# Optimization experiments

Measured on AMD Instinct MI355X. Metric: run time of the kernel, lower is better.

The kernel has to match this reference:

```python
import jax, jax.numpy as jnp
import numpy as np

N_NODES = 100000
N_EDGES = 1000000
HIDDEN = 64
NUM_CONVS = 3
EPS = 0.0  # GINEConv eps, not trained


def setup_inputs() -> dict:
    key = jax.random.key(0)
    ks = jax.random.split(key, 8)
    z = jax.random.randint(ks[0], (N_NODES,), 0, 100, dtype=jnp.int32)
    edge_index = jax.random.randint(ks[1], (2, N_EDGES), 0, N_NODES, dtype=jnp.int32)
    edge_attr = jax.random.normal(ks[2], (N_EDGES, HIDDEN), dtype=jnp.float32)
    node_emb = jax.random.normal(ks[3], (100, HIDDEN), dtype=jnp.float32)
    s = 1.0 / np.sqrt(HIDDEN)
    W1 = jax.random.uniform(ks[4], (NUM_CONVS, HIDDEN, HIDDEN), jnp.float32, -s, s)
    b1 = jax.random.uniform(ks[5], (NUM_CONVS, HIDDEN), jnp.float32, -s, s)
    W2 = jax.random.uniform(ks[6], (NUM_CONVS, HIDDEN, HIDDEN), jnp.float32, -s, s)
    b2 = jax.random.uniform(ks[7], (NUM_CONVS, HIDDEN), jnp.float32, -s, s)
    return {"node_emb": node_emb, "W1": W1, "b1": b1, "W2": W2, "b2": b2,
            "edge_attr": edge_attr, "z": z, "edge_index": edge_index}


def reference(node_emb, W1, b1, W2, b2, edge_attr, z, edge_index):
    x = node_emb[z]  # [N, H]
    src = edge_index[0]  # x_j (source, message sender)
    dst = edge_index[1]  # aggregation target i
    n = x.shape[0]
    for i in range(NUM_CONVS):
        # message: relu(x_j + edge_attr), scatter-add to target nodes
        msg = jax.nn.relu(x[src] + edge_attr)          # [E, H]
        agg = jax.ops.segment_sum(msg, dst, num_segments=n)  # [N, H]
        out = agg + (1.0 + EPS) * x
        # 2-layer MLP: Linear -> relu -> Linear (no act on last layer)
        h = jax.nn.relu(out @ W1[i].T + b1[i])
        h = h @ W2[i].T + b2[i]
        if i < NUM_CONVS - 1:
            h = jax.nn.relu(h)  # encoder-level activation between convs
        h = h + x  # short_cut residual
        x = h
    return x
```

## Files before the change

### kernel.cpp

```cpp
#include <hip/hip_runtime.h>

#define N_NODES 100000
#define N_EDGES 1000000
#define HID 64
#define SCAN_B 1024
#define SCAN_NB ((N_NODES + SCAN_B - 1) / SCAN_B)

__global__ __launch_bounds__(256) void gather_kernel(
    const float* __restrict__ node_emb, const int* __restrict__ z,
    float* __restrict__ x)
{
    int t = blockIdx.x * 256 + threadIdx.x;
    int n = t >> 4, c = t & 15;
    if (n >= N_NODES) return;
    int zi = z[n];
    float4 v = ((const float4*)(node_emb + (size_t)zi * HID))[c];
    ((float4*)(x + (size_t)n * HID))[c] = v;
}

__global__ __launch_bounds__(256) void hist_kernel(
    const int* __restrict__ dst, int* __restrict__ offs)
{
    int e = blockIdx.x * 256 + threadIdx.x;
    if (e < N_EDGES) atomicAdd(&offs[dst[e]], 1);
}

__global__ __launch_bounds__(1024) void scan1_kernel(
    int* __restrict__ offs, int* __restrict__ bsum)
{
    __shared__ int wsum[16];
    int tid = threadIdx.x, lane = tid & 63, wid = tid >> 6;
    int i = blockIdx.x * SCAN_B + tid;
    int v = (i < N_NODES) ? offs[i] : 0;
    int s = v;
#pragma unroll
    for (int d = 1; d < 64; d <<= 1) {
        int t = __shfl_up(s, (unsigned)d, 64);
        if (lane >= d) s += t;
    }
    if (lane == 63) wsum[wid] = s;
    __syncthreads();
    if (wid == 0) {
        int w = (lane < 16) ? wsum[lane] : 0;
#pragma unroll
        for (int d = 1; d < 16; d <<= 1) {
            int t = __shfl_up(w, (unsigned)d, 64);
            if (lane >= d) w += t;
        }
        if (lane < 16) wsum[lane] = w;
    }
    __syncthreads();
    int woff = (wid == 0) ? 0 : wsum[wid - 1];
    if (i < N_NODES) offs[i] = woff + s - v;
    if (tid == 1023) bsum[blockIdx.x] = wsum[15];
}

__global__ __launch_bounds__(128) void scan2_kernel(int* __restrict__ bsum)
{
    __shared__ int ws[2];
    int tid = threadIdx.x, lane = tid & 63, wid = tid >> 6;
    int v = (tid < SCAN_NB) ? bsum[tid] : 0;
    int s = v;
#pragma unroll
    for (int d = 1; d < 64; d <<= 1) {
        int t = __shfl_up(s, (unsigned)d, 64);
        if (lane >= d) s += t;
    }
    if (lane == 63) ws[wid] = s;
    __syncthreads();
    int add = (wid == 1) ? ws[0] : 0;
    if (tid < SCAN_NB) bsum[tid] = add + s - v;
}

__global__ __launch_bounds__(1024) void scan3_kernel(
    int* __restrict__ offs, const int* __restrict__ bsum)
{
    int i = blockIdx.x * SCAN_B + threadIdx.x;
    if (i < N_NODES) {
        int v = offs[i] + bsum[blockIdx.x];
        atomicExch(&offs[i], v);
    }
}

__global__ __launch_bounds__(256) void fill_kernel(
    const int* __restrict__ src, const int* __restrict__ dst,
    int* __restrict__ offs, int2* __restrict__ eid2)
{
    int e = blockIdx.x * 256 + threadIdx.x;
    if (e < N_EDGES) {
        int d = dst[e];
        int pos = atomicAdd(&offs[d], 1);
        eid2[pos] = make_int2(e, src[e]);
    }
}

__global__ __launch_bounds__(256) void sort_kernel(
    const int* __restrict__ offs, int2* __restrict__ eid2)
{
    int gt = blockIdx.x * 256 + threadIdx.x;
    int n = gt >> 6;
    int lane = threadIdx.x & 63;
    if (n >= N_NODES) return;
    int start = (n == 0) ? 0 : offs[n - 1];
    int end = offs[n];
    int deg = end - start;
    if (deg <= 1 || deg > 64) return;
    int ke = 0x7fffffff, vs = 0;
    if (lane < deg) { int2 t = eid2[start + lane]; ke = t.x; vs = t.y; }
#pragma unroll
    for (int k = 2; k <= 64; k <<= 1) {
        for (int j = k >> 1; j > 0; j >>= 1) {
            int partner = lane ^ j;
            int ke2 = __shfl(ke, partner, 64);
            int vs2 = __shfl(vs, partner, 64);
            bool up = ((lane & k) == 0);
            bool takemin = ((lane < partner) == up);
            bool sw = takemin ? (ke2 < ke) : (ke2 > ke);
            if (sw) { ke = ke2; vs = vs2; }
        }
    }
    if (lane < deg) eid2[start + lane] = make_int2(ke, vs);
}

template<int FIRST>
__global__ __launch_bounds__(256) void agg_kernel(
    const float* __restrict__ x, const float* __restrict__ ea,
    float* __restrict__ eap, const int2* __restrict__ eid2,
    int* __restrict__ srcs, const int* __restrict__ offs,
    float* __restrict__ agg)
{
    int gt = blockIdx.x * 256 + threadIdx.x;
    int n = gt >> 6;
    if (n >= N_NODES) return;
    int lane = threadIdx.x & 63;
    int g = lane >> 4, c4 = lane & 15;
    int nu = __builtin_amdgcn_readfirstlane(n);
    int start = (nu == 0) ? 0 : offs[nu - 1];
    int end = offs[nu];
    float4 acc = make_float4(0.f, 0.f, 0.f, 0.f);
    for (int i = start + g; i < end; i += 4) {
        int sidx;
        float4 e4;
        if (FIRST) {
            int2 p = eid2[i];
            sidx = p.y;
            if (c4 == 0) srcs[i] = sidx;
            e4 = ((const float4*)(ea + (size_t)p.x * HID))[c4];
            ((float4*)(eap + (size_t)i * HID))[c4] = e4;
        } else {
            sidx = srcs[i];
            e4 = ((const float4*)(eap + (size_t)i * HID))[c4];
        }
        float4 x4 = ((const float4*)(x + (size_t)sidx * HID))[c4];
        acc.x += fmaxf(x4.x + e4.x, 0.f);
        acc.y += fmaxf(x4.y + e4.y, 0.f);
        acc.z += fmaxf(x4.z + e4.z, 0.f);
        acc.w += fmaxf(x4.w + e4.w, 0.f);
    }
    acc.x += __shfl_xor(acc.x, 16, 64);
    acc.y += __shfl_xor(acc.y, 16, 64);
    acc.z += __shfl_xor(acc.z, 16, 64);
    acc.w += __shfl_xor(acc.w, 16, 64);
    acc.x += __shfl_xor(acc.x, 32, 64);
    acc.y += __shfl_xor(acc.y, 32, 64);
    acc.z += __shfl_xor(acc.z, 32, 64);
    acc.w += __shfl_xor(acc.w, 32, 64);
    if (g == 0) ((float4*)(agg + (size_t)n * HID))[c4] = acc;
}

#define REP16(M) M(0) M(1) M(2) M(3) M(4) M(5) M(6) M(7) \
                 M(8) M(9) M(10) M(11) M(12) M(13) M(14) M(15)

__global__ __launch_bounds__(256, 2) void mlp_kernel(
    const float* __restrict__ agg,
    const float* __restrict__ W1, const float* __restrict__ b1,
    const float* __restrict__ W2, const float* __restrict__ b2,
    float* __restrict__ x, int last_relu)
{
    __shared__ float sW1[HID * HID];
    __shared__ float sW2T[HID * HID];
    __shared__ float sb1[HID];
    int tid = threadIdx.x;
    for (int idx = tid; idx < HID * HID; idx += 256) {
        sW1[idx] = W1[idx];
        int r = idx >> 6, col = idx & 63;
        sW2T[col * HID + r] = W2[idx];
    }
    if (tid < HID) sb1[tid] = b1[tid];
    __syncthreads();

    int n = blockIdx.x * 256 + tid;
    if (n >= N_NODES) return;

    const float4* ap = (const float4*)(agg + (size_t)n * HID);
    const float4* xp = (const float4*)(x + (size_t)n * HID);
    const float4* b2p = (const float4*)b2;

#define DECL_IN(k) float4 in##k; { float4 a = ap[k], b = xp[k]; \
    in##k.x = a.x + b.x; in##k.y = a.y + b.y; \
    in##k.z = a.z + b.z; in##k.w = a.w + b.w; }
    REP16(DECL_IN)
#undef DECL_IN

#define DECL_O(k) float4 o##k = b2p[k];
    REP16(DECL_O)
#undef DECL_O

    for (int j = 0; j < HID; ++j) {
        const float4* w1p = (const float4*)(sW1 + j * HID);
        float a0 = 0.f, a1 = 0.f, a2 = 0.f, a3 = 0.f;
#define DOT4(k, acc) { float4 w = w1p[k]; \
    acc += in##k.x * w.x + in##k.y * w.y + in##k.z * w.z + in##k.w * w.w; }
        DOT4(0, a0)  DOT4(1, a1)  DOT4(2, a2)  DOT4(3, a3)
        DOT4(4, a0)  DOT4(5, a1)  DOT4(6, a2)  DOT4(7, a3)
        DOT4(8, a0)  DOT4(9, a1)  DOT4(10, a2) DOT4(11, a3)
        DOT4(12, a0) DOT4(13, a1) DOT4(14, a2) DOT4(15, a3)
#undef DOT4
        float h = fmaxf((a0 + a1) + (a2 + a3) + sb1[j], 0.f);
        const float4* w2p = (const float4*)(sW2T + j * HID);
#define AXPY(k) { float4 w = w2p[k]; \
    o##k.x += h * w.x; o##k.y += h * w.y; \
    o##k.z += h * w.z; o##k.w += h * w.w; }
        REP16(AXPY)
#undef AXPY
    }

    float4* orow = (float4*)(x + (size_t)n * HID);
#define STORE(k) { float4 xv = xp[k]; float4 r; \
    r.x = (last_relu ? fmaxf(o##k.x, 0.f) : o##k.x) + xv.x; \
    r.y = (last_relu ? fmaxf(o##k.y, 0.f) : o##k.y) + xv.y; \
    r.z = (last_relu ? fmaxf(o##k.z, 0.f) : o##k.z) + xv.z; \
    r.w = (last_relu ? fmaxf(o##k.w, 0.f) : o##k.w) + xv.w; \
    orow[k] = r; }
    REP16(STORE)
#undef STORE
}

extern "C" void kernel_launch(void* const* d_in, const int* in_sizes, int n_in,
                              void* d_out, int out_size, void* d_ws, size_t ws_size,
                              hipStream_t stream) {
    const float* node_emb = (const float*)d_in[0];
    const float* W1 = (const float*)d_in[1];
    const float* b1 = (const float*)d_in[2];
    const float* W2 = (const float*)d_in[3];
    const float* b2 = (const float*)d_in[4];
    const float* ea = (const float*)d_in[5];
    const int* z = (const int*)d_in[6];
    const int* ei = (const int*)d_in[7];
    const int* src = ei;
    const int* dst = ei + N_EDGES;

    float* x = (float*)d_out;
    float* eap = (float*)d_ws;
    float* agg = eap + (size_t)N_EDGES * HID;
    int2* eid2 = (int2*)(agg + (size_t)N_NODES * HID);
    int* offs = (int*)(eid2 + N_EDGES);
    int* bsum = offs + N_NODES;
    int* srcs = bsum + 128;

    const int eb = (N_EDGES + 255) / 256;
    const int gather_blocks = (N_NODES * 16) / 256;
    const int nodewave_blocks = (N_NODES * 64) / 256;
    const int mlp_blocks = (N_NODES + 255) / 256;

    hipMemsetAsync(offs, 0, N_NODES * sizeof(int), stream);
    gather_kernel<<<gather_blocks, 256, 0, stream>>>(node_emb, z, x);
    hist_kernel<<<eb, 256, 0, stream>>>(dst, offs);
    scan1_kernel<<<SCAN_NB, SCAN_B, 0, stream>>>(offs, bsum);
    scan2_kernel<<<1, 128, 0, stream>>>(bsum);
    scan3_kernel<<<SCAN_NB, SCAN_B, 0, stream>>>(offs, bsum);
    fill_kernel<<<eb, 256, 0, stream>>>(src, dst, offs, eid2);
    sort_kernel<<<nodewave_blocks, 256, 0, stream>>>(offs, eid2);

    agg_kernel<1><<<nodewave_blocks, 256, 0, stream>>>(x, ea, eap, eid2, srcs, offs, agg);
    mlp_kernel<<<mlp_blocks, 256, 0, stream>>>(
        agg, W1, b1, W2, b2, x, 1);
    for (int conv = 1; conv < 3; ++conv) {
        agg_kernel<0><<<nodewave_blocks, 256, 0, stream>>>(x, ea, eap, eid2, srcs, offs, agg);
        mlp_kernel<<<mlp_blocks, 256, 0, stream>>>(
            agg, W1 + conv * HID * HID, b1 + conv * HID,
            W2 + conv * HID * HID, b2 + conv * HID,
            x, conv < 2 ? 1 : 0);
    }
}
```

Measured before the change: 992.0 us.

## Drop permuted edge-attr copy; gather edge attrs directly with wave-shuffled indices

Stops materializing a CSR-permuted copy of edge_attr (256MB write plus reread) and the srcs array in the first conv. Every conv now gathers edge_attr rows by original edge id, and the wave loads up to 64 (edge id, src) pairs at once and broadcasts them via shuffles instead of per-iteration index loads. The gather and histogram kernels are also merged into one launch. The cost is random row gathers from edge_attr in all three convs instead of streaming contiguous reads in two of them.

Result: faster. 942.6 us (-5.0%).

```diff
diff --git a/kernel.cpp b/kernel.cpp
--- a/kernel.cpp
+++ b/kernel.cpp
@@ -5,24 +5,24 @@
 #define HID 64
 #define SCAN_B 1024
 #define SCAN_NB ((N_NODES + SCAN_B - 1) / SCAN_B)
-
-__global__ __launch_bounds__(256) void gather_kernel(
+#define GATHER_BLOCKS ((N_NODES * 16) / 256)
+#define HIST_BLOCKS ((N_EDGES + 255) / 256)
+
+__global__ __launch_bounds__(256) void prep_kernel(
     const float* __restrict__ node_emb, const int* __restrict__ z,
-    float* __restrict__ x)
-{
-    int t = blockIdx.x * 256 + threadIdx.x;
-    int n = t >> 4, c = t & 15;
-    if (n >= N_NODES) return;
-    int zi = z[n];
-    float4 v = ((const float4*)(node_emb + (size_t)zi * HID))[c];
-    ((float4*)(x + (size_t)n * HID))[c] = v;
-}
-
-__global__ __launch_bounds__(256) void hist_kernel(
-    const int* __restrict__ dst, int* __restrict__ offs)
-{
-    int e = blockIdx.x * 256 + threadIdx.x;
-    if (e < N_EDGES) atomicAdd(&offs[dst[e]], 1);
+    float* __restrict__ x, const int* __restrict__ dst, int* __restrict__ offs)
+{
+    if (blockIdx.x < GATHER_BLOCKS) {
+        int t = blockIdx.x * 256 + threadIdx.x;
+        int n = t >> 4, c = t & 15;
+        if (n >= N_NODES) return;
+        int zi = z[n];
+        float4 v = ((const float4*)(node_emb + (size_t)zi * HID))[c];
+        ((float4*)(x + (size_t)n * HID))[c] = v;
+    } else {
+        int e = (blockIdx.x - GATHER_BLOCKS) * 256 + threadIdx.x;
+        if (e < N_EDGES) atomicAdd(&offs[dst[e]], 1);
+    }
 }
 
 __global__ __launch_bounds__(1024) void scan1_kernel(
@@ -122,11 +122,9 @@
     if (lane < deg) eid2[start + lane] = make_int2(ke, vs);
 }
 
-template<int FIRST>
 __global__ __launch_bounds__(256) void agg_kernel(
     const float* __restrict__ x, const float* __restrict__ ea,
-    float* __restrict__ eap, const int2* __restrict__ eid2,
-    int* __restrict__ srcs, const int* __restrict__ offs,
+    const int2* __restrict__ eid2, const int* __restrict__ offs,
     float* __restrict__ agg)
 {
     int gt = blockIdx.x * 256 + threadIdx.x;
@@ -137,21 +135,29 @@
     int nu = __builtin_amdgcn_readfirstlane(n);
     int start = (nu == 0) ? 0 : offs[nu - 1];
     int end = offs[nu];
+    int deg = end - start;
+    int2 my = make_int2(0, 0);
+    if (lane < deg) my = eid2[start + lane];
     float4 acc = make_float4(0.f, 0.f, 0.f, 0.f);
-    for (int i = start + g; i < end; i += 4) {
-        int sidx;
-        float4 e4;
-        if (FIRST) {
-            int2 p = eid2[i];
-            sidx = p.y;
-            if (c4 == 0) srcs[i] = sidx;
-            e4 = ((const float4*)(ea + (size_t)p.x * HID))[c4];
-            ((float4*)(eap + (size_t)i * HID))[c4] = e4;
-        } else {
-            sidx = srcs[i];
-            e4 = ((const float4*)(eap + (size_t)i * HID))[c4];
+    int dmax = deg < 64 ? deg : 64;
+    int iters = (dmax + 3) >> 2;
+    for (int j = 0; j < iters; ++j) {
+        int k = g + 4 * j;
+        int eidx = __shfl(my.x, k, 64);
+        int sidx = __shfl(my.y, k, 64);
+        if (k < dmax) {
+            float4 e4 = ((const float4*)(ea + (size_t)eidx * HID))[c4];
+            float4 x4 = ((const float4*)(x + (size_t)sidx * HID))[c4];
+            acc.x += fmaxf(x4.x + e4.x, 0.f);
+            acc.y += fmaxf(x4.y + e4.y, 0.f);
+            acc.z += fmaxf(x4.z + e4.z, 0.f);
+            acc.w += fmaxf(x4.w + e4.w, 0.f);
         }
-        float4 x4 = ((const float4*)(x + (size_t)sidx * HID))[c4];
+    }
+    for (int i = start + 64 + g; i < end; i += 4) {
+        int2 p = eid2[i];
+        float4 e4 = ((const float4*)(ea + (size_t)p.x * HID))[c4];
+        float4 x4 = ((const float4*)(x + (size_t)p.y * HID))[c4];
         acc.x += fmaxf(x4.x + e4.x, 0.f);
         acc.y += fmaxf(x4.y + e4.y, 0.f);
         acc.z += fmaxf(x4.z + e4.z, 0.f);
@@ -251,32 +257,26 @@
     const int* dst = ei + N_EDGES;
 
     float* x = (float*)d_out;
-    float* eap = (float*)d_ws;
-    float* agg = eap + (size_t)N_EDGES * HID;
+    float* agg = (float*)d_ws;
     int2* eid2 = (int2*)(agg + (size_t)N_NODES * HID);
     int* offs = (int*)(eid2 + N_EDGES);
     int* bsum = offs + N_NODES;
-    int* srcs = bsum + 128;
 
     const int eb = (N_EDGES + 255) / 256;
-    const int gather_blocks = (N_NODES * 16) / 256;
     const int nodewave_blocks = (N_NODES * 64) / 256;
     const int mlp_blocks = (N_NODES + 255) / 256;
 
     hipMemsetAsync(offs, 0, N_NODES * sizeof(int), stream);
-    gather_kernel<<<gather_blocks, 256, 0, stream>>>(node_emb, z, x);
-    hist_kernel<<<eb, 256, 0, stream>>>(dst, offs);
+    prep_kernel<<<GATHER_BLOCKS + HIST_BLOCKS, 256, 0, stream>>>(
+        node_emb, z, x, dst, offs);
     scan1_kernel<<<SCAN_NB, SCAN_B, 0, stream>>>(offs, bsum);
     scan2_kernel<<<1, 128, 0, stream>>>(bsum);
     scan3_kernel<<<SCAN_NB, SCAN_B, 0, stream>>>(offs, bsum);
     fill_kernel<<<eb, 256, 0, stream>>>(src, dst, offs, eid2);
     sort_kernel<<<nodewave_blocks, 256, 0, stream>>>(offs, eid2);
 
-    agg_kernel<1><<<nodewave_blocks, 256, 0, stream>>>(x, ea, eap, eid2, srcs, offs, agg);
-    mlp_kernel<<<mlp_blocks, 256, 0, stream>>>(
-        agg, W1, b1, W2, b2, x, 1);
-    for (int conv = 1; conv < 3; ++conv) {
-        agg_kernel<0><<<nodewave_blocks, 256, 0, stream>>>(x, ea, eap, eid2, srcs, offs, agg);
+    for (int conv = 0; conv < 3; ++conv) {
+        agg_kernel<<<nodewave_blocks, 256, 0, stream>>>(x, ea, eid2, offs, agg);
         mlp_kernel<<<mlp_blocks, 256, 0, stream>>>(
             agg, W1 + conv * HID * HID, b1 + conv * HID,
             W2 + conv * HID * HID, b2 + conv * HID,
```
